# Kernel optimization log

Hardware: AMD Instinct MI355X
Metric: run time of the kernel (lower is better)

Reference implementation:

```python
import jax, jax.numpy as jnp
import numpy as np

N_NODES = 50000
N_EDGES = 800000
IN_CH = 128
OUT_CH = 64
HEADS = 1
NEG_SLOPE = 0.2

def _glorot(key, shape):
    stdv = np.sqrt(6.0 / (shape[-2] + shape[-1]))
    return jax.random.uniform(key, shape, jnp.float32, -stdv, stdv)

def setup_inputs() -> dict:
    key = jax.random.key(0)
    k1, k2, k3, k4, k5 = jax.random.split(key, 5)
    x = jax.random.normal(k1, (N_NODES, IN_CH), jnp.float32)
    src = jax.random.randint(k2, (N_EDGES,), 0, N_NODES)
    dst = jax.random.randint(k3, (N_EDGES,), 0, N_NODES)
    # ensure no pre-existing self loops (remove_self_loops is then identity)
    dst = jnp.where(src == dst, (dst + 1) % N_NODES, dst)
    edge_index = jnp.stack([src, dst]).astype(jnp.int64)
    weight = _glorot(k4, (IN_CH, HEADS * OUT_CH))
    att = _glorot(k5, (1, HEADS, 2 * OUT_CH))
    bias = jnp.zeros((OUT_CH,), jnp.float32)
    return {"x": x, "edge_index": edge_index, "weight": weight, "att": att, "bias": bias}

def reference(x, edge_index, weight, att, bias):
    N = x.shape[0]
    # linear projection -> [N, heads, out]
    h = (x @ weight).reshape(N, HEADS, OUT_CH)
    # add self loops (input guaranteed free of self loops)
    loops = jnp.arange(N, dtype=edge_index.dtype)
    src = jnp.concatenate([edge_index[0], loops])  # source j
    dst = jnp.concatenate([edge_index[1], loops])  # target i
    x_j = h[src]   # [E+N, heads, out]
    x_i = h[dst]
    # attention logits: (cat([x_i, x_j]) * att).sum(-1) -> [E+N, heads]
    alpha = jnp.concatenate([x_i, x_j], axis=-1)
    alpha = (alpha * att).sum(axis=-1)
    alpha = jax.nn.leaky_relu(alpha, NEG_SLOPE)
    # segment softmax over destination nodes
    amax = jax.ops.segment_max(alpha, dst, num_segments=N)
    e = jnp.exp(alpha - amax[dst])
    esum = jax.ops.segment_sum(e, dst, num_segments=N)
    alpha = e / (esum[dst] + 1e-16)
    # message + scatter-add aggregation
    msg = x_j * alpha[:, :, None]
    out = jax.ops.segment_sum(msg, dst, num_segments=N)  # [N, heads, out]
    out = out.mean(axis=1) + bias
    # F.normalize (L2, dim=1, eps=1e-12); dropout is eval-mode identity
    norm = jnp.maximum(jnp.linalg.norm(out, axis=1, keepdims=True), 1e-12)
    return out / norm
```

## Files before the change

### kernel.cpp

```cpp
#include <hip/hip_runtime.h>
#include <math.h>

#define IN_CH 128
#define OUT_CH 64
#define NEG_SLOPE 0.2f
#define CAP 64
#define BSHIFT 8
#define BS 256
#define CHUNK_EDGES 4096

typedef long long ll2 __attribute__((ext_vector_type(2)));
typedef int i4v __attribute__((ext_vector_type(4)));

__device__ __forceinline__ unsigned short f2bf(float f) {
    unsigned u = __float_as_uint(f);
    unsigned r = (u + 0x7FFFu + ((u >> 16) & 1u)) >> 16;
    return (unsigned short)r;
}

__device__ __forceinline__ void gload_lds16(const void* g, void* l) {
    __builtin_amdgcn_global_load_lds(
        (const __attribute__((address_space(1))) void*)g,
        (__attribute__((address_space(3))) void*)l, 16, 0, 0);
}

__device__ __forceinline__ bool sniff_is64(const void* edges) {
    const unsigned* up = (const unsigned*)edges;
    bool is64 = true;
#pragma unroll
    for (int k = 0; k < 16; k++) is64 = is64 && (up[2 * k + 1] == 0u);
    return is64;
}

__global__ __launch_bounds__(256) void k_bucket(
        const void* __restrict__ edges, int E, int nbkt,
        int2* __restrict__ bucket, int bcap, int* __restrict__ bucket_cnt) {
    __shared__ int lcur[256];
    __shared__ int lbase[256];
    int t = threadIdx.x;
    lcur[t] = 0;
    __syncthreads();

    int base = blockIdx.x * CHUNK_EDGES + t * 16;
    bool is64 = sniff_is64(edges);
    int sv[16], dv[16], rr[16];
    int nv = E - base;
    if (nv > 16) nv = 16;
    if (nv < 0) nv = 0;
    if (nv == 16) {
        if (is64) {
            const ll2* ps = (const ll2*)((const long long*)edges + base);
            const ll2* pd = (const ll2*)((const long long*)edges + (size_t)E + base);
#pragma unroll
            for (int i = 0; i < 8; i++) {
                ll2 v = __builtin_nontemporal_load(ps + i);
                sv[2 * i] = (int)v.x; sv[2 * i + 1] = (int)v.y;
            }
#pragma unroll
            for (int i = 0; i < 8; i++) {
                ll2 w = __builtin_nontemporal_load(pd + i);
                dv[2 * i] = (int)w.x; dv[2 * i + 1] = (int)w.y;
            }
        } else {
            const i4v* ps = (const i4v*)((const int*)edges + base);
            const i4v* pd = (const i4v*)((const int*)edges + E + base);
#pragma unroll
            for (int i = 0; i < 4; i++) {
                i4v v = __builtin_nontemporal_load(ps + i);
                sv[4 * i] = v.x; sv[4 * i + 1] = v.y;
                sv[4 * i + 2] = v.z; sv[4 * i + 3] = v.w;
            }
#pragma unroll
            for (int i = 0; i < 4; i++) {
                i4v w = __builtin_nontemporal_load(pd + i);
                dv[4 * i] = w.x; dv[4 * i + 1] = w.y;
                dv[4 * i + 2] = w.z; dv[4 * i + 3] = w.w;
            }
        }
    } else {
        for (int i = 0; i < 16; i++) {
            if (i < nv) {
                if (is64) {
                    sv[i] = (int)((const long long*)edges)[base + i];
                    dv[i] = (int)((const long long*)edges)[(size_t)E + base + i];
                } else {
                    sv[i] = ((const int*)edges)[base + i];
                    dv[i] = ((const int*)edges)[E + base + i];
                }
            } else { sv[i] = 0; dv[i] = 0; }
        }
    }
#pragma unroll
    for (int i = 0; i < 16; i++)
        if (i < nv) rr[i] = atomicAdd(&lcur[(unsigned)dv[i] >> BSHIFT], 1);
    __syncthreads();
    if (t < nbkt && lcur[t] > 0) lbase[t] = atomicAdd(bucket_cnt + t, lcur[t]);
    __syncthreads();
#pragma unroll
    for (int i = 0; i < 16; i++) {
        if (i < nv) {
            int b = (unsigned)dv[i] >> BSHIFT;
            bucket[(size_t)b * bcap + lbase[b] + rr[i]] = make_int2(sv[i], dv[i]);
        }
    }
}

__global__ __launch_bounds__(256) void k_mm_cs(
        const float* __restrict__ x, const float* __restrict__ W,
        const float* __restrict__ att, unsigned short* __restrict__ h16,
        float* __restrict__ asrc, float* __restrict__ adst, int N,
        const int2* __restrict__ bucket, int bcap,
        const int* __restrict__ bucket_cnt, int* __restrict__ counts,
        int* __restrict__ slots, int* __restrict__ oflow_cnt,
        int2* __restrict__ oflow, int mmb, int csb) {
    __shared__ float Ws[IN_CH * OUT_CH];
    __shared__ float Xs[64 * IN_CH];
    int t = threadIdx.x;
    int bid = blockIdx.x;
    int total = mmb + csb;
    int cbefore = (int)(((long long)bid * csb) / total);
    int cafter  = (int)(((long long)(bid + 1) * csb) / total);
    bool iscs = (cafter != cbefore);
    int id = iscs ? cbefore : (bid - cbefore);

    if (iscs) {
        int* lcnt = (int*)Ws;
        int lo = id << BSHIFT;
        lcnt[t] = 0;
        __syncthreads();
        int cnt = bucket_cnt[id];
        const int2* mybkt = bucket + (size_t)id * bcap;
        for (int idx = t; idx < cnt; idx += 256) {
            int2 e = mybkt[idx];
            int r = atomicAdd(&lcnt[e.y - lo], 1);
            if (r < CAP) {
                slots[((size_t)e.y << 6) + r] = e.x;
            } else {
                int p2 = atomicAdd(oflow_cnt, 1);
                oflow[p2] = e;
            }
        }
        __syncthreads();
        int node = lo + t;
        if (node < N) counts[node] = lcnt[t];
        return;
    }

    {
        int wv_ = t >> 6;
        int lane = t & 63;
        int col16 = (lane & 31) * 4;
#pragma unroll
        for (int i = 0; i < 8; i++) {
            int seg = wv_ * 8 + i;
            int row = id * 64 + seg * 2 + (lane >> 5);
            row = min(row, N - 1);
            gload_lds16(&x[(size_t)row * IN_CH + col16], &Xs[seg * 256]);
        }
    }
    for (int i = t * 4; i < IN_CH * OUT_CH; i += 256 * 4)
        *(float4*)&Ws[i] = *(const float4*)&W[i];
    int cg = t & 15, g = t >> 4;
    float4 att_d = *(const float4*)&att[cg * 4];
    float4 att_s = *(const float4*)&att[64 + cg * 4];
    __syncthreads();

    int n0 = id * 64 + g * 4;

    float4 acc[4];
#pragma unroll
    for (int m = 0; m < 4; m++) acc[m] = make_float4(0.f, 0.f, 0.f, 0.f);

#pragma unroll 2
    for (int k4 = 0; k4 < IN_CH / 4; k4++) {
        float4 xv[4];
#pragma unroll
        for (int m = 0; m < 4; m++)
            xv[m] = *(const float4*)&Xs[(g * 4 + m) * IN_CH + k4 * 4];
        float4 wv[4];
#pragma unroll
        for (int j = 0; j < 4; j++)
            wv[j] = *(const float4*)&Ws[(k4 * 4 + j) * OUT_CH + cg * 4];
#pragma unroll
        for (int m = 0; m < 4; m++) {
            acc[m].x = fmaf(xv[m].x, wv[0].x, acc[m].x);
            acc[m].y = fmaf(xv[m].x, wv[0].y, acc[m].y);
            acc[m].z = fmaf(xv[m].x, wv[0].z, acc[m].z);
            acc[m].w = fmaf(xv[m].x, wv[0].w, acc[m].w);
            acc[m].x = fmaf(xv[m].y, wv[1].x, acc[m].x);
            acc[m].y = fmaf(xv[m].y, wv[1].y, acc[m].y);
            acc[m].z = fmaf(xv[m].y, wv[1].z, acc[m].z);
            acc[m].w = fmaf(xv[m].y, wv[1].w, acc[m].w);
            acc[m].x = fmaf(xv[m].z, wv[2].x, acc[m].x);
            acc[m].y = fmaf(xv[m].z, wv[2].y, acc[m].y);
            acc[m].z = fmaf(xv[m].z, wv[2].z, acc[m].z);
            acc[m].w = fmaf(xv[m].z, wv[2].w, acc[m].w);
            acc[m].x = fmaf(xv[m].w, wv[3].x, acc[m].x);
            acc[m].y = fmaf(xv[m].w, wv[3].y, acc[m].y);
            acc[m].z = fmaf(xv[m].w, wv[3].z, acc[m].z);
            acc[m].w = fmaf(xv[m].w, wv[3].w, acc[m].w);
        }
    }

#pragma unroll
    for (int m = 0; m < 4; m++) {
        int node = n0 + m;
        if (node < N) {
            ushort4 hv;
            hv.x = f2bf(acc[m].x);
            hv.y = f2bf(acc[m].y);
            hv.z = f2bf(acc[m].z);
            hv.w = f2bf(acc[m].w);
            *(ushort4*)&h16[(size_t)node * OUT_CH + cg * 4] = hv;
        }
        float pd = acc[m].x * att_d.x + acc[m].y * att_d.y +
                   acc[m].z * att_d.z + acc[m].w * att_d.w;
        float ps = acc[m].x * att_s.x + acc[m].y * att_s.y +
                   acc[m].z * att_s.z + acc[m].w * att_s.w;
#pragma unroll
        for (int msk = 1; msk < 16; msk <<= 1) {
            pd += __shfl_xor(pd, msk, 64);
            ps += __shfl_xor(ps, msk, 64);
        }
        if (cg == 0 && node < N) { adst[node] = pd; asrc[node] = ps; }
    }
}

__global__ __launch_bounds__(256) void k_agg(const unsigned short* __restrict__ h16,
                                             const int* __restrict__ slots,
                                             const int* __restrict__ counts,
                                             const int* __restrict__ oflow_cnt,
                                             const int2* __restrict__ oflow,
                                             const float* __restrict__ asrc,
                                             const float* __restrict__ adst,
                                             const float* __restrict__ bias,
                                             float* __restrict__ out, int N) {
    __shared__ float2 stage[4][64];
    int lane = threadIdx.x & 63;
    int wid = threadIdx.x >> 6;
    int node = blockIdx.x * 4 + wid;
    if (node >= N) return;
    int half = lane >> 5;
    int ch2 = (lane & 31) * 2;

    float aD = adst[node];
    float a = aD + asrc[node];
    a = a > 0.f ? a : NEG_SLOPE * a;
    float w_self = __expf(a);
    unsigned hv = *(const unsigned*)&h16[(size_t)node * OUT_CH + ch2];
    float wse = half ? 0.f : w_self;
    float accx = wse * __uint_as_float(hv << 16);
    float accy = wse * __uint_as_float(hv & 0xFFFF0000u);

    int c = counts[node];
    int cs = min(c, CAP);
    int sv = 0;
    float wv = 0.f;
    if (lane < cs) {
        sv = slots[((size_t)node << 6) + lane];
        float av = aD + asrc[sv];
        av = av > 0.f ? av : NEG_SLOPE * av;
        wv = __expf(av);
    }
    float esum_lane = wv;
    stage[wid][lane] = make_float2(__int_as_float(sv), wv);

    for (int j = 0; j < cs; j += 16) {
#pragma unroll
        for (int k = 0; k < 8; k++) {
            float2 p = stage[wid][j + 2 * k + half];
            int s = __float_as_int(p.x);
            unsigned v = *(const unsigned*)&h16[((size_t)s << 6) + ch2];
            accx = fmaf(p.y, __uint_as_float(v << 16), accx);
            accy = fmaf(p.y, __uint_as_float(v & 0xFFFF0000u), accy);
        }
    }
    accx += __shfl_xor(accx, 32, 64);
    accy += __shfl_xor(accy, 32, 64);
#pragma unroll
    for (int m = 32; m >= 1; m >>= 1) esum_lane += __shfl_xor(esum_lane, m, 64);
    float esum = esum_lane + w_self;

    int oc = *oflow_cnt;
    if (oc > 0) {
        for (int i = 0; i < oc; i++) {
            int2 e = oflow[i];
            if (e.y == node) {
                float av = aD + asrc[e.x];
                av = av > 0.f ? av : NEG_SLOPE * av;
                float w = __expf(av);
                esum += w;
                unsigned v = *(const unsigned*)&h16[((size_t)e.x << 6) + ch2];
                accx = fmaf(w, __uint_as_float(v << 16), accx);
                accy = fmaf(w, __uint_as_float(v & 0xFFFF0000u), accy);
            }
        }
    }

    float inv = 1.f / (esum + 1e-16f);
    float2 bv = *(const float2*)&bias[ch2];
    float vx = accx * inv + bv.x;
    float vy = accy * inv + bv.y;
    float ss = vx * vx + vy * vy;
#pragma unroll
    for (int m = 16; m >= 1; m >>= 1) ss += __shfl_xor(ss, m, 64);
    float rinv = 1.f / fmaxf(sqrtf(ss), 1e-12f);
    if (!half)
        *(float2*)&out[(size_t)node * OUT_CH + ch2] = make_float2(vx * rinv, vy * rinv);
}

extern "C" void kernel_launch(void* const* d_in, const int* in_sizes, int n_in,
                              void* d_out, int out_size, void* d_ws, size_t ws_size,
                              hipStream_t stream) {
    const float* x    = (const float*)d_in[0];
    const void*  edges = d_in[1];
    const float* W    = (const float*)d_in[2];
    const float* att  = (const float*)d_in[3];
    const float* bias = (const float*)d_in[4];
    float* out = (float*)d_out;

    const int N = in_sizes[0] / IN_CH;
    const int E = in_sizes[1] / 2;
    const int NBKT = (N + BS - 1) / BS;
    const int MMB = (N + 63) / 64;
    const int BKB = (E + CHUNK_EDGES - 1) / CHUNK_EDGES;
    const int bcap = E / NBKT + 2048;

    char* ws = (char*)d_ws;
    size_t off = 0;
    auto alloc = [&](size_t bytes) -> void* {
        void* p = ws + off;
        off += bytes;
        off = (off + 255) & ~(size_t)255;
        return p;
    };
    int*            ctrl     = (int*)alloc(320 * 4);
    int*            counts   = (int*)alloc((size_t)N * 4);
    int*            slots    = (int*)alloc((size_t)N * CAP * 4);
    int2*           oflow    = (int2*)alloc((size_t)65536 * 8);
    unsigned short* h16      = (unsigned short*)alloc((size_t)N * OUT_CH * 2);
    float*          asrc     = (float*)alloc((size_t)N * 4);
    float*          adst     = (float*)alloc((size_t)N * 4);
    int2*           bucket   = (int2*)alloc((size_t)NBKT * bcap * 8);
    int*            bucket_cnt = ctrl;
    int*            oflow_cnt  = ctrl + 256;

    hipMemsetAsync(ctrl, 0, 320 * 4, stream);
    k_bucket<<<BKB, 256, 0, stream>>>(edges, E, NBKT, bucket, bcap, bucket_cnt);
    k_mm_cs<<<MMB + NBKT, 256, 0, stream>>>(x, W, att, h16, asrc, adst, N,
                                            bucket, bcap, bucket_cnt, counts,
                                            slots, oflow_cnt, oflow, MMB, NBKT);
    k_agg<<<(N + 3) / 4, 256, 0, stream>>>(h16, slots, counts, oflow_cnt, oflow,
                                           asrc, adst, bias, out, N);
}
```

Baseline: 135.6 us.

## Co-schedule edge bucketing with the projection matmul and split slot placement out

```diff
diff --git a/kernel.cpp b/kernel.cpp
--- a/kernel.cpp
+++ b/kernel.cpp
@@ -32,120 +32,88 @@
     return is64;
 }
 
-__global__ __launch_bounds__(256) void k_bucket(
-        const void* __restrict__ edges, int E, int nbkt,
-        int2* __restrict__ bucket, int bcap, int* __restrict__ bucket_cnt) {
-    __shared__ int lcur[256];
-    __shared__ int lbase[256];
-    int t = threadIdx.x;
-    lcur[t] = 0;
-    __syncthreads();
-
-    int base = blockIdx.x * CHUNK_EDGES + t * 16;
-    bool is64 = sniff_is64(edges);
-    int sv[16], dv[16], rr[16];
-    int nv = E - base;
-    if (nv > 16) nv = 16;
-    if (nv < 0) nv = 0;
-    if (nv == 16) {
-        if (is64) {
-            const ll2* ps = (const ll2*)((const long long*)edges + base);
-            const ll2* pd = (const ll2*)((const long long*)edges + (size_t)E + base);
-#pragma unroll
-            for (int i = 0; i < 8; i++) {
-                ll2 v = __builtin_nontemporal_load(ps + i);
-                sv[2 * i] = (int)v.x; sv[2 * i + 1] = (int)v.y;
-            }
-#pragma unroll
-            for (int i = 0; i < 8; i++) {
-                ll2 w = __builtin_nontemporal_load(pd + i);
-                dv[2 * i] = (int)w.x; dv[2 * i + 1] = (int)w.y;
-            }
-        } else {
-            const i4v* ps = (const i4v*)((const int*)edges + base);
-            const i4v* pd = (const i4v*)((const int*)edges + E + base);
-#pragma unroll
-            for (int i = 0; i < 4; i++) {
-                i4v v = __builtin_nontemporal_load(ps + i);
-                sv[4 * i] = v.x; sv[4 * i + 1] = v.y;
-                sv[4 * i + 2] = v.z; sv[4 * i + 3] = v.w;
-            }
-#pragma unroll
-            for (int i = 0; i < 4; i++) {
-                i4v w = __builtin_nontemporal_load(pd + i);
-                dv[4 * i] = w.x; dv[4 * i + 1] = w.y;
-                dv[4 * i + 2] = w.z; dv[4 * i + 3] = w.w;
-            }
-        }
-    } else {
-        for (int i = 0; i < 16; i++) {
-            if (i < nv) {
-                if (is64) {
-                    sv[i] = (int)((const long long*)edges)[base + i];
-                    dv[i] = (int)((const long long*)edges)[(size_t)E + base + i];
-                } else {
-                    sv[i] = ((const int*)edges)[base + i];
-                    dv[i] = ((const int*)edges)[E + base + i];
-                }
-            } else { sv[i] = 0; dv[i] = 0; }
-        }
-    }
-#pragma unroll
-    for (int i = 0; i < 16; i++)
-        if (i < nv) rr[i] = atomicAdd(&lcur[(unsigned)dv[i] >> BSHIFT], 1);
-    __syncthreads();
-    if (t < nbkt && lcur[t] > 0) lbase[t] = atomicAdd(bucket_cnt + t, lcur[t]);
-    __syncthreads();
-#pragma unroll
-    for (int i = 0; i < 16; i++) {
-        if (i < nv) {
-            int b = (unsigned)dv[i] >> BSHIFT;
-            bucket[(size_t)b * bcap + lbase[b] + rr[i]] = make_int2(sv[i], dv[i]);
-        }
-    }
-}
-
-__global__ __launch_bounds__(256) void k_mm_cs(
+__global__ __launch_bounds__(256) void k_mm_bkt(
         const float* __restrict__ x, const float* __restrict__ W,
         const float* __restrict__ att, unsigned short* __restrict__ h16,
         float* __restrict__ asrc, float* __restrict__ adst, int N,
-        const int2* __restrict__ bucket, int bcap,
-        const int* __restrict__ bucket_cnt, int* __restrict__ counts,
-        int* __restrict__ slots, int* __restrict__ oflow_cnt,
-        int2* __restrict__ oflow, int mmb, int csb) {
-    __shared__ float Ws[IN_CH * OUT_CH];
+        const void* __restrict__ edges, int E, int nbkt,
+        int2* __restrict__ bucket, int bcap, int* __restrict__ bucket_cnt) {
     __shared__ float Xs[64 * IN_CH];
     int t = threadIdx.x;
     int bid = blockIdx.x;
-    int total = mmb + csb;
-    int cbefore = (int)(((long long)bid * csb) / total);
-    int cafter  = (int)(((long long)(bid + 1) * csb) / total);
-    bool iscs = (cafter != cbefore);
-    int id = iscs ? cbefore : (bid - cbefore);
-
-    if (iscs) {
-        int* lcnt = (int*)Ws;
-        int lo = id << BSHIFT;
-        lcnt[t] = 0;
+
+    if (bid < nbkt) {
+        int* lcur = (int*)Xs;
+        int* lbase = lcur + 256;
+        lcur[t] = 0;
         __syncthreads();
-        int cnt = bucket_cnt[id];
-        const int2* mybkt = bucket + (size_t)id * bcap;
-        for (int idx = t; idx < cnt; idx += 256) {
-            int2 e = mybkt[idx];
-            int r = atomicAdd(&lcnt[e.y - lo], 1);
-            if (r < CAP) {
-                slots[((size_t)e.y << 6) + r] = e.x;
+
+        int base = bid * CHUNK_EDGES + t * 16;
+        bool is64 = sniff_is64(edges);
+        int sv[16], dv[16], rr[16];
+        int nv = E - base;
+        if (nv > 16) nv = 16;
+        if (nv < 0) nv = 0;
+        if (nv == 16) {
+            if (is64) {
+                const ll2* ps = (const ll2*)((const long long*)edges + base);
+                const ll2* pd = (const ll2*)((const long long*)edges + (size_t)E + base);
+#pragma unroll
+                for (int i = 0; i < 8; i++) {
+                    ll2 v = __builtin_nontemporal_load(ps + i);
+                    sv[2 * i] = (int)v.x; sv[2 * i + 1] = (int)v.y;
+                }
+#pragma unroll
+                for (int i = 0; i < 8; i++) {
+                    ll2 w = __builtin_nontemporal_load(pd + i);
+                    dv[2 * i] = (int)w.x; dv[2 * i + 1] = (int)w.y;
+                }
             } else {
-                int p2 = atomicAdd(oflow_cnt, 1);
-                oflow[p2] = e;
+                const i4v* ps = (const i4v*)((const int*)edges + base);
+                const i4v* pd = (const i4v*)((const int*)edges + E + base);
+#pragma unroll
+                for (int i = 0; i < 4; i++) {
+                    i4v v = __builtin_nontemporal_load(ps + i);
+                    sv[4 * i] = v.x; sv[4 * i + 1] = v.y;
+                    sv[4 * i + 2] = v.z; sv[4 * i + 3] = v.w;
+                }
+#pragma unroll
+                for (int i = 0; i < 4; i++) {
+                    i4v w = __builtin_nontemporal_load(pd + i);
+                    dv[4 * i] = w.x; dv[4 * i + 1] = w.y;
+                    dv[4 * i + 2] = w.z; dv[4 * i + 3] = w.w;
+                }
             }
-        }
+        } else {
+            for (int i = 0; i < 16; i++) {
+                if (i < nv) {
+                    if (is64) {
+                        sv[i] = (int)((const long long*)edges)[base + i];
+                        dv[i] = (int)((const long long*)edges)[(size_t)E + base + i];
+                    } else {
+                        sv[i] = ((const int*)edges)[base + i];
+                        dv[i] = ((const int*)edges)[E + base + i];
+                    }
+                } else { sv[i] = 0; dv[i] = 0; }
+            }
+        }
+#pragma unroll
+        for (int i = 0; i < 16; i++)
+            if (i < nv) rr[i] = atomicAdd(&lcur[(unsigned)dv[i] >> BSHIFT], 1);
         __syncthreads();
-        int node = lo + t;
-        if (node < N) counts[node] = lcnt[t];
+        if (t < nbkt && lcur[t] > 0) lbase[t] = atomicAdd(bucket_cnt + t, lcur[t]);
+        __syncthreads();
+#pragma unroll
+        for (int i = 0; i < 16; i++) {
+            if (i < nv) {
+                int b = (unsigned)dv[i] >> BSHIFT;
+                bucket[(size_t)b * bcap + lbase[b] + rr[i]] = make_int2(sv[i], dv[i]);
+            }
+        }
         return;
     }
 
+    int id = bid - nbkt;
     {
         int wv_ = t >> 6;
         int lane = t & 63;
@@ -158,8 +126,6 @@
             gload_lds16(&x[(size_t)row * IN_CH + col16], &Xs[seg * 256]);
         }
     }
-    for (int i = t * 4; i < IN_CH * OUT_CH; i += 256 * 4)
-        *(float4*)&Ws[i] = *(const float4*)&W[i];
     int cg = t & 15, g = t >> 4;
     float4 att_d = *(const float4*)&att[cg * 4];
     float4 att_s = *(const float4*)&att[64 + cg * 4];
@@ -180,7 +146,7 @@
         float4 wv[4];
 #pragma unroll
         for (int j = 0; j < 4; j++)
-            wv[j] = *(const float4*)&Ws[(k4 * 4 + j) * OUT_CH + cg * 4];
+            wv[j] = *(const float4*)&W[(k4 * 4 + j) * OUT_CH + cg * 4];
 #pragma unroll
         for (int m = 0; m < 4; m++) {
             acc[m].x = fmaf(xv[m].x, wv[0].x, acc[m].x);
@@ -226,6 +192,34 @@
     }
 }
 
+__global__ __launch_bounds__(256) void k_cs(
+        const int2* __restrict__ bucket, int bcap,
+        const int* __restrict__ bucket_cnt, int* __restrict__ counts,
+        int* __restrict__ slots, int* __restrict__ oflow_cnt,
+        int2* __restrict__ oflow, int N) {
+    __shared__ int lcnt[256];
+    int t = threadIdx.x;
+    int id = blockIdx.x;
+    int lo = id << BSHIFT;
+    lcnt[t] = 0;
+    __syncthreads();
+    int cnt = bucket_cnt[id];
+    const int2* mybkt = bucket + (size_t)id * bcap;
+    for (int idx = t; idx < cnt; idx += 256) {
+        int2 e = mybkt[idx];
+        int r = atomicAdd(&lcnt[e.y - lo], 1);
+        if (r < CAP) {
+            slots[((size_t)e.y << 6) + r] = e.x;
+        } else {
+            int p2 = atomicAdd(oflow_cnt, 1);
+            oflow[p2] = e;
+        }
+    }
+    __syncthreads();
+    int node = lo + t;
+    if (node < N) counts[node] = lcnt[t];
+}
+
 __global__ __launch_bounds__(256) void k_agg(const unsigned short* __restrict__ h16,
                                              const int* __restrict__ slots,
                                              const int* __restrict__ counts,
@@ -324,6 +318,7 @@
     const int NBKT = (N + BS - 1) / BS;
     const int MMB = (N + 63) / 64;
     const int BKB = (E + CHUNK_EDGES - 1) / CHUNK_EDGES;
+    const int K1B = (BKB > NBKT ? BKB : NBKT);
     const int bcap = E / NBKT + 2048;
 
     char* ws = (char*)d_ws;
@@ -346,10 +341,11 @@
     int*            oflow_cnt  = ctrl + 256;
 
     hipMemsetAsync(ctrl, 0, 320 * 4, stream);
-    k_bucket<<<BKB, 256, 0, stream>>>(edges, E, NBKT, bucket, bcap, bucket_cnt);
-    k_mm_cs<<<MMB + NBKT, 256, 0, stream>>>(x, W, att, h16, asrc, adst, N,
-                                            bucket, bcap, bucket_cnt, counts,
-                                            slots, oflow_cnt, oflow, MMB, NBKT);
+    k_mm_bkt<<<K1B + MMB, 256, 0, stream>>>(x, W, att, h16, asrc, adst, N,
+                                            edges, E, NBKT, bucket, bcap,
+                                            bucket_cnt);
+    k_cs<<<NBKT, 256, 0, stream>>>(bucket, bcap, bucket_cnt, counts,
+                                   slots, oflow_cnt, oflow, N);
     k_agg<<<(N + 3) / 4, 256, 0, stream>>>(h16, slots, counts, oflow_cnt, oflow,
                                            asrc, adst, bias, out, N);
 }
```

Measured after the change: 137.6 us. No clear change (+1.5%).
